# Kernel tuning notes

Measured on AMD Instinct MI355X. Metric: run time of the kernel, lower is better.

Reference implementation:

```python
import jax, jax.numpy as jnp
import numpy as np
from jax import lax

B, C, H, W = 2, 3, 112, 112
PERCENTILE = 95.0


def setup_inputs() -> dict:
    key = jax.random.key(0)
    kx, ky = jax.random.split(key)
    x = jax.random.normal(kx, (B, C, H, W), dtype=jnp.float32)
    y = jax.random.randint(ky, (B, H, W), 0, C)
    return {"x": x, "y": y}


def _masked_quantile(vals, mask, q):
    # torch.quantile (linear interpolation) over entries of `vals` where mask is True.
    n = jnp.sum(mask)
    s = jnp.sort(jnp.where(mask, vals, jnp.inf))  # valid entries first, inf-padded
    pos = q * jnp.maximum(n - 1, 0).astype(vals.dtype)
    lo = jnp.floor(pos).astype(jnp.int32)
    hi = jnp.ceil(pos).astype(jnp.int32)
    frac = pos - lo.astype(vals.dtype)
    v = s[lo] * (1.0 - frac) + s[hi] * frac
    return jnp.where(n > 0, v, jnp.zeros((), vals.dtype))


def _forward(x, y):
    b, c = x.shape[0], x.shape[1]
    n = H * W
    pred = jnp.argmax(x, axis=1).reshape(b, n)   # [b, N] predicted labels
    gt = y.reshape(b, n).astype(pred.dtype)      # [b, N] gt labels

    # voxel coordinates of the full grid; nonzero() point sets become boolean masks over it
    ii, jj = jnp.meshgrid(jnp.arange(H, dtype=jnp.float32),
                          jnp.arange(W, dtype=jnp.float32), indexing="ij")
    coords = jnp.stack([ii.ravel(), jj.ravel()], axis=1)  # [N, 2]
    sq = jnp.sum(coords * coords, axis=1)
    d2 = sq[:, None] + sq[None, :] - 2.0 * (coords @ coords.T)
    D = jnp.sqrt(jnp.maximum(d2, 0.0))  # [N, N] symmetric all-pairs voxel distances

    cls = jnp.arange(c, dtype=pred.dtype)
    seg_masks = (pred[:, None, :] == cls[None, :, None]).reshape(b * c, n)  # [b*c, N]
    gt_masks = (gt[:, None, :] == cls[None, :, None]).reshape(b * c, n)
    q = jnp.float32(PERCENTILE / 100.0)

    def one(masks):
        seg_m, gt_m = masks
        # min distance from every voxel to the gt / seg point set
        d_to_gt = jnp.min(jnp.where(gt_m[None, :], D, jnp.inf), axis=1)   # [N]
        d_to_seg = jnp.min(jnp.where(seg_m[None, :], D, jnp.inf), axis=1)  # [N]
        hd1 = _masked_quantile(d_to_gt, seg_m, q)   # over seg points
        hd2 = _masked_quantile(d_to_seg, gt_m, q)   # over gt points
        hd = jnp.maximum(hd1, hd2)
        ok = (jnp.sum(seg_m) > 0) & (jnp.sum(gt_m) > 0)  # empty set -> 0.0
        return jnp.where(ok, hd, jnp.zeros((), D.dtype))

    hd_vals = lax.map(one, (seg_masks, gt_masks))  # sequential over b*c pairs, one [N,N] temp at a time
    return jnp.mean(hd_vals)


def reference(x, y):
    return _forward(x, y)
```

## Files before the change

### kernel.cpp

```cpp
#include <hip/hip_runtime.h>

#define BB 2
#define CC 3
#define HH 112
#define WW 112
#define NN (HH*WW)
#define NPAIR (BB*CC)
#define NCOMBO (NPAIR*2)
#define NBINS 24643
#define HWORDS ((NBINS+1)/2)
#define INF29 (1<<29)
#define RCH 8
#define NCHUNK (HH/RCH)
#define NTHR 1024
#define NQ4 (NN/4)
#define NFW2 (NN/32)
#define NOQ 0xFFFFFFFFu
#define POISON 0xAAAAAAAAu
#define CSTRIDE 16
#define CTR_INTS ((NCOMBO+1)*CSTRIDE)

typedef unsigned long long ull;

__device__ __forceinline__ int predLab3(float a, float b, float d) {
    int lab = 0; float best = a;
    if (b > best) { best = b; lab = 1; }
    if (d > best) lab = 2;
    return lab;
}
__device__ __forceinline__ void sinku(unsigned v) { asm volatile("" :: "v"(v)); }
__device__ __forceinline__ void sinkf(float v)    { asm volatile("" :: "v"(v)); }

union Smem {
    struct {
        unsigned flatU[NFW2];
        unsigned colQ[4][WW];
        int G[RCH][WW];
    } ab;
    unsigned hist[HWORDS];
};

__global__ __launch_bounds__(NTHR) void fused_kernel(
        const float* __restrict__ x, const int* __restrict__ yl,
        unsigned* __restrict__ d2g, unsigned* __restrict__ ctrs,
        float* __restrict__ qvalg, float* __restrict__ out) {
    __shared__ Smem sm;
    __shared__ int wsum[NTHR/64];
    __shared__ float vlh[2];
    __shared__ int lastFlag, gLastFlag;
    __shared__ float rq[NCOMBO];

    const int tid = threadIdx.x;
    const int m     = blockIdx.x / NCHUNK;
    const int chunk = blockIdx.x % NCHUNK;
    const int r0 = chunk * RCH;
    const int pair = m >> 1, src = m & 1;
    const int b = pair / CC, c = pair % CC;
    const float* xb = x + (size_t)b * CC * NN;
    const int*   yb = yl + b * NN;
    unsigned* d2m  = d2g + m * NN;
    unsigned* ctr  = ctrs + m * CSTRIDE;
    unsigned* done = ctrs + NCOMBO * CSTRIDE;

    for (int i = tid; i < NFW2; i += NTHR) sm.ab.flatU[i] = 0u;
    __syncthreads();

    #pragma unroll
    for (int k = 0; k < (NQ4 + NTHR - 1) / NTHR; k++) {
        int t4 = k * NTHR + tid;
        if (t4 < NQ4) {
            int v4 = t4 * 4;
            unsigned nib;
            if (src) {
                const float4 a  = *(const float4*)(xb + v4);
                const float4 b4 = *(const float4*)(xb + NN + v4);
                const float4 d4 = *(const float4*)(xb + 2 * NN + v4);
                nib  = (unsigned)(predLab3(a.x, b4.x, d4.x) == c);
                nib |= (unsigned)(predLab3(a.y, b4.y, d4.y) == c) << 1;
                nib |= (unsigned)(predLab3(a.z, b4.z, d4.z) == c) << 2;
                nib |= (unsigned)(predLab3(a.w, b4.w, d4.w) == c) << 3;
            } else {
                const int4 yv = *(const int4*)(yb + v4);
                nib  = (unsigned)(yv.x == c) | ((unsigned)(yv.y == c) << 1)
                     | ((unsigned)(yv.z == c) << 2) | ((unsigned)(yv.w == c) << 3);
            }
            if (nib) atomicOr(&sm.ab.flatU[t4 >> 3], nib << ((t4 & 7) << 2));
        }
    }
    __syncthreads();

    if (tid < 4 * WW) {
        int xcolT = tid % WW, q = tid / WW;
        int jmax = (q == 3) ? (HH - 96) : 32;
        unsigned acc = 0;
        int p = (q * 32) * WW + xcolT;
        for (int j = 0; j < jmax; j++) {
            acc |= ((sm.ab.flatU[p >> 5] >> (p & 31)) & 1u) << j;
            p += WW;
        }
        sm.ab.colQ[q][xcolT] = acc;
    }
    __syncthreads();

    const int xcol = tid % WW, rsel = tid / WW;
    const bool act = (tid < RCH * WW);

    if (act) {
        ull lo64 = sm.ab.colQ[0][xcol] | ((ull)sm.ab.colQ[1][xcol] << 32);
        ull hi64 = sm.ab.colQ[2][xcol] | ((ull)sm.ab.colQ[3][xcol] << 32);
        int r = r0 + rsel;
        ull mleLo, mleHi, mgeLo, mgeHi;
        if (r < 64) {
            mleLo = (2ull << r) - 1;  mleHi = 0;
            mgeLo = ~((1ull << r) - 1); mgeHi = ~0ull;
        } else {
            int rr = r - 64;
            mleLo = ~0ull; mleHi = (2ull << rr) - 1;
            mgeLo = 0;     mgeHi = ~((1ull << rr) - 1);
        }
        ull sL = lo64 & mleLo, sH = hi64 & mleHi;
        ull tL = lo64 & mgeLo, tH = hi64 & mgeHi;
        int posUp = sH ? (127 - (int)__builtin_clzll(sH))
                       : (sL ? (63 - (int)__builtin_clzll(sL)) : -4000);
        int posDn = tL ? (int)__builtin_ctzll(tL)
                       : (tH ? 64 + (int)__builtin_ctzll(tH) : 8000);
        int d = min(r - posUp, posDn - r);
        sm.ab.G[rsel][xcol] = d * d;
    }
    __syncthreads();

    if (act) {
        int a0 = INF29, a1 = INF29, a2 = INF29, a3 = INF29;
        #pragma unroll 4
        for (int xx = 0; xx < WW; xx += 4) {
            int d0 = xcol - xx, d1 = xcol - xx - 1, d2v = xcol - xx - 2, d3 = xcol - xx - 3;
            a0 = min(a0, d0 * d0   + sm.ab.G[rsel][xx]);
            a1 = min(a1, d1 * d1   + sm.ab.G[rsel][xx + 1]);
            a2 = min(a2, d2v * d2v + sm.ab.G[rsel][xx + 2]);
            a3 = min(a3, d3 * d3   + sm.ab.G[rsel][xx + 3]);
        }
        int dreg = min(min(a0, a1), min(a2, a3));
        int v = (r0 + rsel) * WW + xcol;
        int qlab = src ? yb[v] : predLab3(xb[v], xb[NN + v], xb[2 * NN + v]);
        unsigned val = (qlab == c) ? (unsigned)min(dreg, NBINS - 1) : NOQ;
        sinku(atomicExch(&d2m[v], val));
    }
    __syncthreads();

    if (tid == 0) {
        unsigned prev = atomicAdd(ctr, 1u);
        if (prev >= POISON) prev -= POISON;
        lastFlag = (prev == NCHUNK - 1);
    }
    __syncthreads();
    if (!lastFlag) return;
    if (tid == 0) atomicExch(ctr, 0u);

    for (int i = tid; i < HWORDS; i += NTHR) sm.hist[i] = 0u;
    __syncthreads();
    #pragma unroll
    for (int k = 0; k < (NN + NTHR - 1) / NTHR; k++) {
        int i = k * NTHR + tid;
        if (i < NN) {
            unsigned d2 = atomicAdd(&d2m[i], 0u);
            if (d2 != NOQ) atomicAdd(&sm.hist[d2 >> 1], 1u << ((d2 & 1) << 4));
        }
    }
    __syncthreads();

    const int CHUNKB = (NBINS + NTHR - 1) / NTHR;
    int lo = tid * CHUNKB, hiE = min(lo + CHUNKB, NBINS);
    int s = 0;
    for (int i = lo; i < hiE; i++) s += (sm.hist[i >> 1] >> ((i & 1) << 4)) & 0xffff;

    const int lane = tid & 63, wid = tid >> 6;
    int incl = s;
    #pragma unroll
    for (int o = 1; o < 64; o <<= 1) {
        int t2 = __shfl_up(incl, o, 64);
        if (lane >= o) incl += t2;
    }
    if (lane == 63) wsum[wid] = incl;
    __syncthreads();
    if (wid == 0) {
        int vv = (lane < NTHR / 64) ? wsum[lane] : 0;
        #pragma unroll
        for (int o = 1; o < NTHR / 64; o <<= 1) {
            int t2 = __shfl_up(vv, o, 64);
            if (lane >= o) vv += t2;
        }
        if (lane < NTHR / 64) wsum[lane] = vv;
    }
    __syncthreads();
    incl += (wid > 0) ? wsum[wid - 1] : 0;
    int excl = incl - s;
    int n = wsum[NTHR / 64 - 1];

    float qv = 0.f;
    if (n > 0) {
        float pos  = 0.95f * (float)(n - 1);
        int   klo  = (int)floorf(pos);
        int   khi  = (int)ceilf(pos);
        float frac = pos - (float)klo;
        #pragma unroll
        for (int which = 0; which < 2; which++) {
            int r = which ? khi : klo;
            if (r >= excl && r < incl) {
                int cacc = excl;
                for (int i = lo; i < hiE; i++) {
                    cacc += (sm.hist[i >> 1] >> ((i & 1) << 4)) & 0xffff;
                    if (cacc > r) { vlh[which] = sqrtf((float)i); break; }
                }
            }
        }
        __syncthreads();
        qv = vlh[0] * (1.f - frac) + vlh[1] * frac;
    }

    if (tid == 0) sinkf(atomicExch(&qvalg[m], (n > 0) ? qv : -1.0f));
    __syncthreads();
    if (tid == 0) {
        unsigned prev = atomicAdd(done, 1u);
        if (prev >= POISON) prev -= POISON;
        gLastFlag = (prev == NCOMBO - 1);
    }
    __syncthreads();
    if (!gLastFlag) return;
    if (tid == 0) atomicExch(done, 0u);

    if (tid < NCOMBO) rq[tid] = atomicAdd(&qvalg[tid], 0.f);
    __syncthreads();
    if (tid == 0) {
        float ssum = 0.f;
        for (int p = 0; p < NPAIR; p++) {
            float a = rq[2 * p], b2 = rq[2 * p + 1];
            float hd = (a >= 0.f && b2 >= 0.f) ? fmaxf(a, b2) : 0.f;
            ssum += hd;
        }
        out[0] = ssum / (float)NPAIR;
    }
}

extern "C" void kernel_launch(void* const* d_in, const int* in_sizes, int n_in,
                              void* d_out, int out_size, void* d_ws, size_t ws_size,
                              hipStream_t stream) {
    const float* x = (const float*)d_in[0];
    const int*   y = (const int*)d_in[1];
    float* out = (float*)d_out;

    unsigned* ws    = (unsigned*)d_ws;
    unsigned* ctrs  = ws;
    unsigned* d2g   = ctrs + CTR_INTS;
    float*    qvalg = (float*)(d2g + NCOMBO * NN);

    fused_kernel<<<NCOMBO * NCHUNK, NTHR, 0, stream>>>(x, y, d2g, ctrs, qvalg, out);
}
```

Before: 21.42 us.

## Compact query distances via ballot/atomic offsets and privatize low histogram bins

Instead of writing every voxel's distance (with a sentinel for non-query voxels) to global memory, each block uses wave ballots and a per-combo atomic counter to write only query-voxel distances into a compacted array. The last block then reads only the n compacted entries, and low-valued bins (most frequent) go into per-wave sub-histograms merged afterwards, reducing shared atomic contention. This adds an extra global atomic and syncs per block, and makes the output order nondeterministic, though that does not affect the histogram.

```diff
diff --git a/kernel.cpp b/kernel.cpp
--- a/kernel.cpp
+++ b/kernel.cpp
@@ -13,12 +13,14 @@
 #define RCH 8
 #define NCHUNK (HH/RCH)
 #define NTHR 1024
+#define ACT_WAVES 14
+#define LOWB 1024
+#define LOWW (LOWB/2)
 #define NQ4 (NN/4)
 #define NFW2 (NN/32)
-#define NOQ 0xFFFFFFFFu
 #define POISON 0xAAAAAAAAu
 #define CSTRIDE 16
-#define CTR_INTS ((NCOMBO+1)*CSTRIDE)
+#define CTR_INTS ((2*NCOMBO+1)*CSTRIDE)
 
 typedef unsigned long long ull;
 
@@ -37,14 +39,19 @@
         unsigned colQ[4][WW];
         int G[RCH][WW];
     } ab;
-    unsigned hist[HWORDS];
+    struct {
+        unsigned hist[HWORDS];
+        unsigned subh[16][LOWW];
+    } ld;
 };
 
 __global__ __launch_bounds__(NTHR) void fused_kernel(
         const float* __restrict__ x, const int* __restrict__ yl,
-        unsigned* __restrict__ d2g, unsigned* __restrict__ ctrs,
+        unsigned* __restrict__ d2c, unsigned* __restrict__ ctrs,
         float* __restrict__ qvalg, float* __restrict__ out) {
     __shared__ Smem sm;
+    __shared__ unsigned wcnt[ACT_WAVES], wbase[ACT_WAVES];
+    __shared__ unsigned blockBase, nSh;
     __shared__ int wsum[NTHR/64];
     __shared__ float vlh[2];
     __shared__ int lastFlag, gLastFlag;
@@ -58,9 +65,10 @@
     const int b = pair / CC, c = pair % CC;
     const float* xb = x + (size_t)b * CC * NN;
     const int*   yb = yl + b * NN;
-    unsigned* d2m  = d2g + m * NN;
-    unsigned* ctr  = ctrs + m * CSTRIDE;
-    unsigned* done = ctrs + NCOMBO * CSTRIDE;
+    unsigned* d2cm = d2c + m * NN;
+    unsigned* ctr  = ctrs + (2*m    ) * CSTRIDE;
+    unsigned* rctr = ctrs + (2*m + 1) * CSTRIDE;
+    unsigned* done = ctrs + (2*NCOMBO) * CSTRIDE;
 
     for (int i = tid; i < NFW2; i += NTHR) sm.ab.flatU[i] = 0u;
     __syncthreads();
@@ -103,6 +111,7 @@
     __syncthreads();
 
     const int xcol = tid % WW, rsel = tid / WW;
+    const int lane = tid & 63, wid = tid >> 6;
     const bool act = (tid < RCH * WW);
 
     if (act) {
@@ -129,6 +138,8 @@
     }
     __syncthreads();
 
+    unsigned val = 0;
+    bool isQ = false;
     if (act) {
         int a0 = INF29, a1 = INF29, a2 = INF29, a3 = INF29;
         #pragma unroll 4
@@ -142,8 +153,29 @@
         int dreg = min(min(a0, a1), min(a2, a3));
         int v = (r0 + rsel) * WW + xcol;
         int qlab = src ? yb[v] : predLab3(xb[v], xb[NN + v], xb[2 * NN + v]);
-        unsigned val = (qlab == c) ? (unsigned)min(dreg, NBINS - 1) : NOQ;
-        sinku(atomicExch(&d2m[v], val));
+        isQ = (qlab == c);
+        val = (unsigned)min(dreg, NBINS - 1);
+    }
+
+    ull wmask = 0;
+    if (act) {
+        wmask = __ballot(isQ);
+        if (lane == 0) wcnt[wid] = (unsigned)__popcll(wmask);
+    }
+    __syncthreads();
+    if (tid == 0) {
+        unsigned t = 0;
+        #pragma unroll
+        for (int w = 0; w < ACT_WAVES; w++) { wbase[w] = t; t += wcnt[w]; }
+        unsigned prev = atomicAdd(rctr, t);
+        if (prev >= POISON) prev -= POISON;
+        blockBase = prev;
+    }
+    __syncthreads();
+    if (act && isQ) {
+        ull below = (1ull << lane) - 1ull;
+        unsigned idx = blockBase + wbase[wid] + (unsigned)__popcll(wmask & below);
+        sinku(atomicExch(&d2cm[idx], val));
     }
     __syncthreads();
 
@@ -154,26 +186,39 @@
     }
     __syncthreads();
     if (!lastFlag) return;
-    if (tid == 0) atomicExch(ctr, 0u);
-
-    for (int i = tid; i < HWORDS; i += NTHR) sm.hist[i] = 0u;
-    __syncthreads();
-    #pragma unroll
-    for (int k = 0; k < (NN + NTHR - 1) / NTHR; k++) {
+    if (tid == 0) {
+        atomicExch(ctr, 0u);
+        unsigned nv = atomicExch(rctr, 0u);
+        if (nv >= POISON) nv -= POISON;
+        nSh = nv;
+    }
+    __syncthreads();
+    const int n = (int)nSh;
+
+    for (int i = tid; i < HWORDS; i += NTHR) sm.ld.hist[i] = 0u;
+    for (int i = tid; i < 16 * LOWW; i += NTHR) ((unsigned*)sm.ld.subh)[i] = 0u;
+    __syncthreads();
+    for (int k = 0; k * NTHR < n; k++) {
         int i = k * NTHR + tid;
-        if (i < NN) {
-            unsigned d2 = atomicAdd(&d2m[i], 0u);
-            if (d2 != NOQ) atomicAdd(&sm.hist[d2 >> 1], 1u << ((d2 & 1) << 4));
-        }
+        if (i < n) {
+            unsigned d2 = atomicAdd(&d2cm[i], 0u);
+            if (d2 < LOWB) atomicAdd(&sm.ld.subh[wid][d2 >> 1], 1u << ((d2 & 1) << 4));
+            else           atomicAdd(&sm.ld.hist[d2 >> 1], 1u << ((d2 & 1) << 4));
+        }
+    }
+    __syncthreads();
+    if (tid < LOWW) {
+        unsigned acc = 0;
+        #pragma unroll
+        for (int w = 0; w < 16; w++) acc += sm.ld.subh[w][tid];
+        sm.ld.hist[tid] += acc;
     }
     __syncthreads();
 
     const int CHUNKB = (NBINS + NTHR - 1) / NTHR;
     int lo = tid * CHUNKB, hiE = min(lo + CHUNKB, NBINS);
     int s = 0;
-    for (int i = lo; i < hiE; i++) s += (sm.hist[i >> 1] >> ((i & 1) << 4)) & 0xffff;
-
-    const int lane = tid & 63, wid = tid >> 6;
+    for (int i = lo; i < hiE; i++) s += (sm.ld.hist[i >> 1] >> ((i & 1) << 4)) & 0xffff;
     int incl = s;
     #pragma unroll
     for (int o = 1; o < 64; o <<= 1) {
@@ -194,7 +239,6 @@
     __syncthreads();
     incl += (wid > 0) ? wsum[wid - 1] : 0;
     int excl = incl - s;
-    int n = wsum[NTHR / 64 - 1];
 
     float qv = 0.f;
     if (n > 0) {
@@ -208,7 +252,7 @@
             if (r >= excl && r < incl) {
                 int cacc = excl;
                 for (int i = lo; i < hiE; i++) {
-                    cacc += (sm.hist[i >> 1] >> ((i & 1) << 4)) & 0xffff;
+                    cacc += (sm.ld.hist[i >> 1] >> ((i & 1) << 4)) & 0xffff;
                     if (cacc > r) { vlh[which] = sqrtf((float)i); break; }
                 }
             }
@@ -250,8 +294,8 @@
 
     unsigned* ws    = (unsigned*)d_ws;
     unsigned* ctrs  = ws;
-    unsigned* d2g   = ctrs + CTR_INTS;
-    float*    qvalg = (float*)(d2g + NCOMBO * NN);
-
-    fused_kernel<<<NCOMBO * NCHUNK, NTHR, 0, stream>>>(x, y, d2g, ctrs, qvalg, out);
+    unsigned* d2c   = ctrs + CTR_INTS;
+    float*    qvalg = (float*)(d2c + NCOMBO * NN);
+
+    fused_kernel<<<NCOMBO * NCHUNK, NTHR, 0, stream>>>(x, y, d2c, ctrs, qvalg, out);
 }
```

After: 21.70 us. Within noise of the previous version (+1.3%).
